# Performance work log

Hardware: AMD Instinct MI355X
Metric: run time of the kernel (lower is better)

The kernel has to match this reference:

```python
import jax, jax.numpy as jnp
import numpy as np

I_CH, O_CH = 64, 64
N_NODES, N_EDGES = 20000, 120000


def build_indices(edge_index):
    """Host-side (numpy) replication of the data-dependent index pipeline:
    sort-by-src -> triplets via searchsorted/repeat_interleave -> sort-by-src ->
    prune low-degree half of nodes -> group-by-src (for scatter-mean) -> reindex.
    All shapes depend only on the (constant) int edge_index.
    """
    ei = np.asarray(edge_index)
    ei = ei[:, np.argsort(ei[0], kind='stable')]
    src, tgt = ei[0], ei[1]
    order = np.argsort(tgt, kind='stable')
    stg = tgt[order]
    lb = np.searchsorted(stg, src, side='left')
    ub = np.searchsorted(stg, src, side='right')
    counts = ub - lb
    T = int(counts.sum())
    rep = np.repeat(np.arange(src.shape[0]), counts)
    start = np.cumsum(counts) - counts
    off = np.arange(T) - start[rep]
    hit = order[lb[rep] + off]
    # triplet rows: (SRC[ALL], TGT[ALL], TGT[R])
    tri = np.stack([src[hit], tgt[hit], tgt[rep]])  # [3, T]
    tri = tri[:, np.argsort(tri[0], kind='stable')]
    # remove(): drop edges touching the lowest-degree half of nodes
    deg = np.bincount(tri.ravel())
    low = np.argsort(deg, kind='stable')[: deg.shape[0] // 2]
    keep = np.ones(deg.shape[0], dtype=bool)
    keep[low] = False
    mask = keep[tri[0]] & keep[tri[1]] & keep[tri[2]]
    pos = np.nonzero(mask)[0]
    tri_kept = tri[:, pos]
    # sum(): group kept triplet-edges by source node
    uniq, inv = np.unique(tri_kept[0], return_inverse=True)
    cnt = np.bincount(inv).astype(np.float32)
    # reindex edge_index to compact node ids
    _, new = np.unique(tri_kept, return_inverse=True)
    new_ei = new.reshape(tri_kept.shape).astype(np.int32)
    return tri.astype(np.int32), pos.astype(np.int32), inv.astype(np.int32), int(uniq.shape[0]), cnt, new_ei


def setup_inputs() -> dict:
    key = jax.random.key(0)
    k1, k2, k3, k4 = jax.random.split(key, 4)
    x = jax.random.normal(k1, (N_NODES, I_CH), dtype=jnp.float32)
    edge_index = jax.random.randint(k2, (2, N_EDGES), 0, N_NODES, dtype=jnp.int32)
    # Conv2d(I, O, (3,1)) parameters
    W = 0.05 * jax.random.normal(k3, (O_CH, I_CH, 3, 1), dtype=jnp.float32)
    b = 0.05 * jax.random.normal(k4, (O_CH,), dtype=jnp.float32)
    return {"x": x, "edge_index": edge_index, "W": W, "b": b}


def reference(x, edge_index, W, b):
    tri, pos, inv, U, cnt, new_ei = build_indices(edge_index)
    tri_j = jnp.asarray(tri)
    # gather: INPUT[i,k,t] = x[tri[k,t], i]  -> g is [3, T, I]
    g = x[tri_j]
    # Conv2d(I,O,(3,1)) on [I,3,T] -> [O,1,T]; squeeze the H dim:
    C = jnp.einsum('oik,kti->ot', W[..., 0], g) + b[:, None]  # [O, T]
    Ck = C[:, jnp.asarray(pos)]  # prune edges touching low-degree nodes
    # scatter-mean over destination group (source node of triplet)
    S = jax.ops.segment_sum(Ck.T, jnp.asarray(inv), num_segments=U)  # [U, O]
    x_new = S / jnp.asarray(cnt)[:, None]
    return x_new, jnp.asarray(new_ei)
```

## Files before the change

kernel.cpp:

```cpp
#include <hip/hip_runtime.h>
#include <stdint.h>

typedef uint32_t u32;
typedef unsigned long long u64;

#define LB_TILE 2048
#define OW_TILE 1024
#define RUN 32

#define S_MAXT 1
#define S_DSTAR 2
#define S_NEED 3
#define S_U 5

__global__ void scan_lb(const u32* __restrict__ in, u32* __restrict__ out, int n,
                        u64* __restrict__ desc){
  __shared__ u32 sh[256];
  __shared__ u32 shPrefix;
  int tid=threadIdx.x, t=blockIdx.x;
  int base = t*LB_TILE + tid*8;
  u32 v[8]; u32 s=0;
#pragma unroll
  for(int k=0;k<8;k++){ u32 xv=(base+k<n)?in[base+k]:0u; v[k]=s; s+=xv; }
  sh[tid]=s; __syncthreads();
  for(int o=1;o<256;o<<=1){
    u32 y=(tid>=o)?sh[tid-o]:0u;
    __syncthreads();
    sh[tid]+=y;
    __syncthreads();
  }
  u32 tileEx = (tid==0)?0u:sh[tid-1];
  u32 agg = sh[255];
  if(tid==0){
    u32 prefix=0u;
    if(t==0){
      atomicExch(&desc[0], ((u64)agg<<32)|2ull);
    } else {
      atomicExch(&desc[t], ((u64)agg<<32)|1ull);
      int j=t-1;
      while(true){
        u64 d=atomicAdd(&desc[j],0ull);
        u32 st=(u32)d;
        if(st==0u) continue;
        prefix += (u32)(d>>32);
        if(st==2u) break;
        --j;
      }
      atomicExch(&desc[t], ((u64)(prefix+agg)<<32)|2ull);
    }
    shPrefix=prefix;
  }
  __syncthreads();
  u32 p=shPrefix+tileEx;
#pragma unroll
  for(int k=0;k<8;k++){ if(base+k<n) out[base+k]=p+v[k]; }
}

__global__ __launch_bounds__(256) void ow_pass(const u64* __restrict__ in,
    u64* __restrict__ outk, const u32* __restrict__ gbase, u64* __restrict__ desc,
    int shift, int hostN, const u32* __restrict__ dCount, int cap){
  __shared__ u32 hist[256], bd[256], cnt2[256];
  __shared__ u32 cnt4[4][256];
  int n = (hostN>=0)?hostN:(int)((*dCount)<(u32)cap?(*dCount):(u32)cap);
  int tid=threadIdx.x, b=blockIdx.x, w=tid>>6, lane=tid&63;
  int base=b*OW_TILE;
  hist[tid]=0u; cnt2[tid]=0u;
  cnt4[0][tid]=0u; cnt4[1][tid]=0u; cnt4[2][tid]=0u; cnt4[3][tid]=0u;
  __syncthreads();
  u64 k[4]; bool act[4];
#pragma unroll
  for(int i=0;i<4;i++){
    int p=base+i*256+tid; act[i]=(p<n);
    k[i]=act[i]?in[p]:0ull;
    if(act[i]) atomicAdd(&hist[(u32)(k[i]>>shift)&255u],1u);
  }
  __syncthreads();
  u32 agg=hist[tid];
  if(b==0){
    atomicExch(&desc[tid], ((u64)agg<<32)|2ull);
    bd[tid]=gbase[tid];
  } else {
    atomicExch(&desc[(size_t)b*256+tid], ((u64)agg<<32)|1ull);
    u32 pre=0u; int j=b-1;
    while(true){
      u64 d=atomicAdd(&desc[(size_t)j*256+tid],0ull);
      u32 st=(u32)d;
      if(st==0u) continue;
      pre+=(u32)(d>>32);
      if(st==2u) break;
      --j;
    }
    atomicExch(&desc[(size_t)b*256+tid], ((u64)(pre+agg)<<32)|2ull);
    bd[tid]=gbase[tid]+pre;
  }
  __syncthreads();
#pragma unroll
  for(int i=0;i<4;i++){
    u32 dig=(u32)(k[i]>>shift)&255u;
    u64 m=__ballot(act[i]?1:0);
    for(int bb=0;bb<8;bb++){
      u64 bl=__ballot((int)((dig>>bb)&1u));
      m &= ((dig>>bb)&1u)?bl:~bl;
    }
    u32 rb=(u32)__popcll(m&((1ull<<lane)-1ull));
    if(act[i]&&rb==0u) cnt4[w][dig]=(u32)__popcll(m);
    __syncthreads();
    if(act[i]){
      u32 off=cnt2[dig]+rb;
      for(int w2=0;w2<w;w2++) off+=cnt4[w2][dig];
      outk[bd[dig]+off]=k[i];
    }
    __syncthreads();
    cnt2[tid]+=cnt4[0][tid]+cnt4[1][tid]+cnt4[2][tid]+cnt4[3][tid];
    cnt4[0][tid]=0u; cnt4[1][tid]=0u; cnt4[2][tid]=0u; cnt4[3][tid]=0u;
    __syncthreads();
  }
}

__global__ void k_prehistE(const u64* __restrict__ keys, u32* __restrict__ hg, int n){
  __shared__ u32 h[4][256];
  int tid=threadIdx.x;
  for(int i=0;i<4;i++) h[i][tid]=0u;
  __syncthreads();
#pragma unroll
  for(int i=0;i<4;i++){
    int p=blockIdx.x*OW_TILE+i*256+tid;
    if(p<n){
      u64 key=keys[p];
      atomicAdd(&h[0][(u32)(key>>24)&255u],1u);
      atomicAdd(&h[1][(u32)(key>>32)&255u],1u);
      atomicAdd(&h[2][(u32)(key>>40)&255u],1u);
      atomicAdd(&h[3][(u32)(key>>48)&255u],1u);
    }
  }
  __syncthreads();
  for(int i=0;i<4;i++) if(h[i][tid]) atomicAdd(&hg[i*256+tid],h[i][tid]);
}

__global__ void k_prehistT(const u64* __restrict__ keys, u32* __restrict__ hg,
                           const u32* __restrict__ dCount, int cap){
  __shared__ u32 h[2][256];
  int n=(int)((*dCount)<(u32)cap?(*dCount):(u32)cap);
  int tid=threadIdx.x;
  h[0][tid]=0u; h[1][tid]=0u;
  __syncthreads();
#pragma unroll
  for(int i=0;i<4;i++){
    int p=blockIdx.x*OW_TILE+i*256+tid;
    if(p<n){
      u64 key=keys[p];
      atomicAdd(&h[0][(u32)(key>>30)&255u],1u);
      atomicAdd(&h[1][(u32)(key>>38)&255u],1u);
    }
  }
  __syncthreads();
  if(h[0][tid]) atomicAdd(&hg[tid],h[0][tid]);
  if(h[1][tid]) atomicAdd(&hg[256+tid],h[1][tid]);
}

__global__ void k_scan256(const u32* __restrict__ hg, u32* __restrict__ gb, int H){
  __shared__ u32 sh[256];
  int t=threadIdx.x;
  for(int hh=0;hh<H;hh++){
    u32 v=hg[hh*256+t];
    sh[t]=v; __syncthreads();
    for(int o=1;o<256;o<<=1){
      u32 y=(t>=o)?sh[t-o]:0u; __syncthreads();
      sh[t]+=y; __syncthreads();
    }
    gb[hh*256+t]=sh[t]-v;
    __syncthreads();
  }
}

__global__ void k_edge0(const u32* __restrict__ src, const u32* __restrict__ tgt,
                        u32* cntS, u32* cntT, u64* keyA, int E){
  int j=blockIdx.x*256+threadIdx.x;
  if(j>=E) return;
  u32 s=src[j], t=tgt[j];
  atomicAdd(&cntS[s],1u); atomicAdd(&cntT[t],1u);
  keyA[j]=((u64)t<<40)|((u64)s<<24)|(u64)j;
}

__global__ void k_deg2m(const u32* __restrict__ src, const u32* __restrict__ tgt,
                        const u32* __restrict__ cntS, const u32* __restrict__ cntT,
                        u32* deg, int* scal, int E){
  __shared__ int mx;
  if(threadIdx.x==0) mx=-1;
  __syncthreads();
  int e=blockIdx.x*256+threadIdx.x;
  int loc=-1;
  if(e<E){
    u32 s=src[e], t=tgt[e];
    u32 w0=cntS[t], w2=cntT[s];
    if(w0){ atomicAdd(&deg[s],w0); loc=(int)(s>t?s:t); }
    if(w2){ atomicAdd(&deg[t],w2); if((int)t>loc) loc=(int)t; }
  }
  if(loc>=0) atomicMax(&mx,loc);
  __syncthreads();
  if(threadIdx.x==0 && mx>=0) atomicMax(&scal[S_MAXT],mx);
}

__global__ void k_degNodeHist(const u32* __restrict__ cntS, const u32* __restrict__ cntT,
                              u32* deg, u32* dh, int NN, const int* __restrict__ scal){
  int v=blockIdx.x*256+threadIdx.x;
  if(v>=NN) return;
  u32 d=deg[v]+cntS[v]*cntT[v];
  deg[v]=d;
  if(v<=scal[S_MAXT]){ if(d>65535u)d=65535u; atomicAdd(&dh[d],1u); }
}

__global__ void k_dstar1b(const u32* __restrict__ dh, int* scal){
  __shared__ u32 part[256];
  __shared__ u32 sc[256];
  int t=threadIdx.x;
  long long kk=(((long long)scal[S_MAXT])+1)>>1;
  u32 s=0;
  for(int i=0;i<256;i++) s+=dh[t*256+i];
  part[t]=s; sc[t]=s; __syncthreads();
  for(int o=1;o<256;o<<=1){
    u32 y=(t>=o)?sc[t-o]:0u; __syncthreads();
    sc[t]+=y; __syncthreads();
  }
  if(kk==0){ if(t==0){ scal[S_DSTAR]=-1; scal[S_NEED]=0; } return; }
  long long cum=(long long)(sc[t]-part[t]);
  if(kk-1>=cum && kk-1<cum+(long long)part[t]){
    long long c=cum;
    for(int i=0;i<256;i++){
      u32 h=dh[t*256+i];
      if(kk-1>=c && kk-1<c+(long long)h){ scal[S_DSTAR]=t*256+i; scal[S_NEED]=(int)(kk-c); break; }
      c+=h;
    }
  }
}

__global__ void k_ef(const u32* __restrict__ deg, u32* ef, int NN, const int* __restrict__ scal){
  int v=blockIdx.x*256+threadIdx.x;
  if(v>NN) return;
  ef[v] = (v<NN && v<=scal[S_MAXT] && (int)deg[v]==scal[S_DSTAR]) ? 1u:0u;
}

__global__ void k_keep(const u32* __restrict__ deg, const u32* __restrict__ rankEq,
                       u32* keep, int NN, const int* __restrict__ scal){
  int v=blockIdx.x*256+threadIdx.x;
  if(v>=NN) return;
  int d=(int)deg[v]; int ds=scal[S_DSTAR]; int need=scal[S_NEED];
  u32 kp=1u;
  if(d<ds) kp=0u;
  else if(d==ds && (int)rankEq[v]<need) kp=0u;
  keep[v]=kp;
}

__global__ void k_keptCnt(const u32* __restrict__ src, const u32* __restrict__ tgt,
                          const u32* __restrict__ keep, u32* kc, int E){
  int j=blockIdx.x*256+threadIdx.x;
  if(j<E && keep[src[j]]) atomicAdd(&kc[tgt[j]],1u);
}

__global__ void k_cntk(const u64* __restrict__ C, const u32* __restrict__ keep,
                       const u32* __restrict__ keptCnt, u32* cntk, int E){
  int e=blockIdx.x*256+threadIdx.x;
  if(e>E) return;
  if(e==E){ cntk[e]=0u; return; }
  u64 ke=C[e];
  u32 s=(u32)(ke>>24)&0xFFFFu, te=(u32)(ke>>40);
  cntk[e]=(keep[s]&keep[te])?keptCnt[s]:0u;
}

__global__ void k_gen_trik(const u64* __restrict__ C, const u64* __restrict__ H,
    const u32* __restrict__ rp_tgt, const u32* __restrict__ keep,
    const u32* __restrict__ startk, u64* __restrict__ trig, int E, int cap){
  int e=blockIdx.x*256+threadIdx.x;
  if(e>=E) return;
  u32 c0=startk[e], c1=startk[e+1];
  if(c0>=c1) return;
  u64 ke=C[e];
  u32 s=(u32)(ke>>24)&0xFFFFu, te=(u32)(ke>>40);
  u32 lb=rp_tgt[s], ub=rp_tgt[s+1];
  u32 idx=c0;
  for(u32 i=lb;i<ub&&idx<c1;++i){
    u64 hk=H[i];
    u32 hsv=(u32)(hk>>24)&0xFFFFu;
    if(keep[hsv]){
      if(idx<(u32)cap) trig[idx]=((u64)hsv<<30)|((u64)s<<15)|(u64)te;
      ++idx;
    }
  }
}

__global__ void k_heads_present(const u64* __restrict__ tri, u32* __restrict__ hf,
    u32* __restrict__ present, const u32* __restrict__ dCount, int KC){
  int Tk=(int)((*dCount)<(u32)KC?(*dCount):(u32)KC);
  int q=blockIdx.x*256+threadIdx.x;
  if(q>KC) return;
  u32 f=0u;
  if(q<Tk){
    u64 key=tri[q];
    f=(q==0||(key>>30)!=(tri[q-1]>>30))?1u:0u;
    present[key>>30]=1u;
    present[(key>>15)&0x7FFFu]=1u;
    present[key&0x7FFFu]=1u;
  }
  hf[q]=f;
}

__global__ void k_gs_ei(const u64* __restrict__ tri, const u32* __restrict__ hf,
    const u32* __restrict__ hsAll, u32* __restrict__ gs, float* __restrict__ out,
    int* scal, const u32* __restrict__ dCount, int KC, int out_size){
  int Tk=(int)((*dCount)<(u32)KC?(*dCount):(u32)KC);
  u32 U=hsAll[KC+1];
  int q=blockIdx.x*256+threadIdx.x;
  if(q==0){ scal[S_U]=(int)U; gs[U]=(u32)Tk; }
  if(q>=Tk) return;
  if(hf[q]) gs[hsAll[q+1]-1u]=(u32)q;
  u64 key=tri[q];
  int bs=(int)U*64;
  int i0=bs+q, i1=bs+Tk+q, i2=bs+2*Tk+q;
  if(i0<out_size) out[i0]=(float)(hsAll[(size_t)KC+1+(size_t)(key>>30)]-U);
  if(i1<out_size) out[i1]=(float)(hsAll[(size_t)KC+1+(size_t)((key>>15)&0x7FFFu)]-U);
  if(i2<out_size) out[i2]=(float)(hsAll[(size_t)KC+1+(size_t)(key&0x7FFFu)]-U);
}

__global__ __launch_bounds__(256) void k_xsum(const float* __restrict__ x,
    const u64* __restrict__ tri, const u32* __restrict__ hs,
    float* __restrict__ S1, float* __restrict__ S2,
    const u32* __restrict__ dCount, int KC){
  int Tk=(int)((*dCount)<(u32)KC?(*dCount):(u32)KC);
  int w=threadIdx.x>>6, lane=threadIdx.x&63;
  int r=blockIdx.x*4+w;
  int q0=r*RUN; if(q0>=Tk) return;
  int q1=q0+RUN; if(q1>Tk)q1=Tk;
  int gcur=(int)hs[q0+1]-1;
  float a1=0.f,a2=0.f;
  for(int q=q0;q<q1;q++){
    int g=(int)hs[q+1]-1;
    if(g!=gcur){
      atomicAdd(&S1[(size_t)gcur*64+lane],a1);
      atomicAdd(&S2[(size_t)gcur*64+lane],a2);
      a1=0.f;a2=0.f;gcur=g;
    }
    u64 key=tri[q];
    a1+=x[(size_t)((key>>15)&0x7FFFull)*64+lane];
    a2+=x[(size_t)(key&0x7FFFull)*64+lane];
  }
  atomicAdd(&S1[(size_t)gcur*64+lane],a1);
  atomicAdd(&S2[(size_t)gcur*64+lane],a2);
}

__global__ __launch_bounds__(256) void k_xmat(const float* __restrict__ x,
    const float* __restrict__ W, const float* __restrict__ b,
    const u64* __restrict__ tri, const u32* __restrict__ gs,
    const float* __restrict__ S1, const float* __restrict__ S2,
    float* __restrict__ out, const int* __restrict__ scal){
  __shared__ float Wl[192*65];
  __shared__ float sv[4][192];
  int tid=threadIdx.x;
  for(int j=tid;j<12288;j+=256){
    int r=j%192, o=j/192;
    Wl[r*65+o]=W[j];
  }
  __syncthreads();
  int U=scal[S_U];
  int w=tid>>6, lane=tid&63;
  float bv=b[lane];
  for(int g=blockIdx.x*4+w; g<U; g+=gridDim.x*4){
    u32 q0=gs[g], q1=gs[g+1];
    u32 uniq=(u32)(tri[q0]>>30);
    sv[w][lane]=x[(size_t)uniq*64+lane];
    sv[w][64+lane]=S1[(size_t)g*64+lane];
    sv[w][128+lane]=S2[(size_t)g*64+lane];
    float acc0=0.f, acc12=0.f;
#pragma unroll 4
    for(int ii=0;ii<64;ii++){
      acc0  += Wl[(ii*3+0)*65+lane]*sv[w][ii];
      acc12 += Wl[(ii*3+1)*65+lane]*sv[w][64+ii]
             + Wl[(ii*3+2)*65+lane]*sv[w][128+ii];
    }
    out[(size_t)g*64+lane] = bv + acc0 + acc12/(float)(q1-q0);
  }
}

extern "C" void kernel_launch(void* const* d_in, const int* in_sizes, int n_in,
                              void* d_out, int out_size, void* d_ws, size_t ws_size,
                              hipStream_t stream){
  const float* x = (const float*)d_in[0];
  const int*   ei = (const int*)d_in[1];
  const float* W = (const float*)d_in[2];
  const float* b = (const float*)d_in[3];
  int NN = in_sizes[0]/64;
  int E  = in_sizes[1]/2;
  const u32* src=(const u32*)ei;
  const u32* tgt=(const u32*)(ei+E);

  int KC = ((out_size/3 + OW_TILE-1)/OW_TILE)*OW_TILE; if(KC<OW_TILE) KC=OW_TILE;
  int B_E=(E+OW_TILE-1)/OW_TILE;
  int B_T=KC/OW_TILE;

  char* base=(char*)d_ws; size_t off=0;
  auto alloc=[&](size_t nInts)->u32*{
    u32* p=(u32*)(base+off);
    off += ( (nInts*4 + 255) & ~(size_t)255 );
    return p;
  };
  int* scal=(int*)alloc(64);
  u32* cntT=alloc(NN+1); u32* cntS=alloc(NN);
  u32* deg=alloc(NN); u32* degHist=alloc(65536);
  u32* keptCnt=alloc(NN);
  u32* histGE=alloc(4*256); u32* histGT=alloc(2*256);
  u64* descS=(u64*)alloc(2*1024);
  u64* descE=(u64*)alloc(2*(size_t)(4*B_E*256));
  u64* descT=(u64*)alloc(2*(size_t)(2*B_T*256));
  u32* hfp=alloc((size_t)KC+1+NN+1);
  float* S1=(float*)alloc((size_t)NN*64);
  float* S2=(float*)alloc((size_t)NN*64);
  size_t zoneBytes = off;
  u64* bufA=(u64*)alloc(2*(size_t)E);
  u64* bufB=(u64*)alloc(2*(size_t)E);
  u64* bufC=(u64*)alloc(2*(size_t)E);
  u64* triA=(u64*)alloc(2*(size_t)KC); u64* triB=(u64*)alloc(2*(size_t)KC);
  u32* rp_tgt=alloc(NN+1);
  u32* cntk=alloc(E+1); u32* startk=alloc(E+1);
  u32* gbaseE=alloc(4*256); u32* gbaseT=alloc(2*256);
  u32* ef=alloc(NN+1); u32* rankEq=alloc(NN+1); u32* keep=alloc(NN);
  u32* gs=alloc(NN+2);
  u32* hsAll=alloc((size_t)KC+1+NN+1);
  if(off > ws_size) return;

  u32* hf=hfp; u32* present=hfp+(KC+1);
  const u32* dCount=startk+E;

  size_t descUsed=0;
  auto scan_ex=[&](const u32* in, u32* out, int n){
    int nb=(n+LB_TILE-1)/LB_TILE;
    scan_lb<<<nb,256,0,stream>>>(in,out,n,descS+descUsed);
    descUsed += (size_t)nb;
  };

  int gE=(E+255)/256, gE1=(E+256)/256;
  int gNN=(NN+255)/256, gNN1=(NN+256)/256;
  int gKC=(KC+255)/256, gKC1=(KC+256)/256;

  hipMemsetAsync(base,0,zoneBytes,stream);

  k_edge0<<<gE,256,0,stream>>>(src,tgt,cntS,cntT,bufA,E);
  k_deg2m<<<gE,256,0,stream>>>(src,tgt,cntS,cntT,deg,scal,E);
  k_degNodeHist<<<gNN,256,0,stream>>>(cntS,cntT,deg,degHist,NN,scal);
  k_dstar1b<<<1,256,0,stream>>>(degHist,scal);
  k_ef<<<gNN1,256,0,stream>>>(deg,ef,NN,scal);
  scan_ex(ef,rankEq,NN+1);
  k_keep<<<gNN,256,0,stream>>>(deg,rankEq,keep,NN,scal);
  k_keptCnt<<<gE,256,0,stream>>>(src,tgt,keep,keptCnt,E);
  scan_ex(cntT,rp_tgt,NN+1);

  k_prehistE<<<B_E,256,0,stream>>>(bufA,histGE,E);
  k_scan256<<<1,256,0,stream>>>(histGE,gbaseE,4);
  ow_pass<<<B_E,256,0,stream>>>(bufA,bufB,gbaseE+0*256,descE+(size_t)0*B_E*256,24,E,nullptr,0);
  ow_pass<<<B_E,256,0,stream>>>(bufB,bufC,gbaseE+1*256,descE+(size_t)1*B_E*256,32,E,nullptr,0);
  ow_pass<<<B_E,256,0,stream>>>(bufC,bufA,gbaseE+2*256,descE+(size_t)2*B_E*256,40,E,nullptr,0);
  ow_pass<<<B_E,256,0,stream>>>(bufA,bufB,gbaseE+3*256,descE+(size_t)3*B_E*256,48,E,nullptr,0);

  k_cntk<<<gE1,256,0,stream>>>(bufC,keep,keptCnt,cntk,E);
  scan_ex(cntk,startk,E+1);
  k_gen_trik<<<gE,256,0,stream>>>(bufC,bufB,rp_tgt,keep,startk,triA,E,KC);

  k_prehistT<<<B_T,256,0,stream>>>(triA,histGT,dCount,KC);
  k_scan256<<<1,256,0,stream>>>(histGT,gbaseT,2);
  ow_pass<<<B_T,256,0,stream>>>(triA,triB,gbaseT+0*256,descT+(size_t)0*B_T*256,30,-1,dCount,KC);
  ow_pass<<<B_T,256,0,stream>>>(triB,triA,gbaseT+1*256,descT+(size_t)1*B_T*256,38,-1,dCount,KC);

  k_heads_present<<<gKC1,256,0,stream>>>(triA,hf,present,dCount,KC);
  scan_ex(hfp,hsAll,KC+1+NN+1);
  float* outF=(float*)d_out;
  k_gs_ei<<<gKC,256,0,stream>>>(triA,hf,hsAll,gs,outF,scal,dCount,KC,out_size);

  k_xsum<<<KC/(4*RUN),256,0,stream>>>(x,triA,hsAll,S1,S2,dCount,KC);
  k_xmat<<<768,256,0,stream>>>(x,W,b,triA,gs,S1,S2,outF,scal);
}
```

Before: 337.3 us.

## Shrink edge sort keys to 32 bits and derive radix bases from degree counts

Edge sort keys are packed as 32-bit (src<<16|tgt) instead of 64-bit keys that carried the edge index, which halves traffic in the four edge radix passes. Global digit bases come from the per-node src/tgt counts via a new k_gbase4 kernel, and the triplet histogram is built inside k_gen_trik, so the separate prehistogram kernels are dropped. The two exclusive scans are merged into one over a concatenated buffer, and radix and scan tiles grow to 4096 elements per block. The trade-offs are that edge order becomes non-stable (the index is no longer in the key), node ids must fit in 16 bits, and larger tiles mean fewer blocks and more registers per thread.

```diff
diff --git a/kernel.cpp b/kernel.cpp
--- a/kernel.cpp
+++ b/kernel.cpp
@@ -4,8 +4,8 @@
 typedef uint32_t u32;
 typedef unsigned long long u64;
 
-#define LB_TILE 2048
-#define OW_TILE 1024
+#define LB_TILE 4096
+#define OW_TILE 4096
 #define RUN 32
 
 #define S_MAXT 1
@@ -18,10 +18,10 @@
   __shared__ u32 sh[256];
   __shared__ u32 shPrefix;
   int tid=threadIdx.x, t=blockIdx.x;
-  int base = t*LB_TILE + tid*8;
-  u32 v[8]; u32 s=0;
+  int base = t*LB_TILE + tid*16;
+  u32 v[16]; u32 s=0;
 #pragma unroll
-  for(int k=0;k<8;k++){ u32 xv=(base+k<n)?in[base+k]:0u; v[k]=s; s+=xv; }
+  for(int k=0;k<16;k++){ u32 xv=(base+k<n)?in[base+k]:0u; v[k]=s; s+=xv; }
   sh[tid]=s; __syncthreads();
   for(int o=1;o<256;o<<=1){
     u32 y=(tid>=o)?sh[tid-o]:0u;
@@ -53,26 +53,25 @@
   __syncthreads();
   u32 p=shPrefix+tileEx;
 #pragma unroll
-  for(int k=0;k<8;k++){ if(base+k<n) out[base+k]=p+v[k]; }
-}
-
-__global__ __launch_bounds__(256) void ow_pass(const u64* __restrict__ in,
-    u64* __restrict__ outk, const u32* __restrict__ gbase, u64* __restrict__ desc,
-    int shift, int hostN, const u32* __restrict__ dCount, int cap){
+  for(int k=0;k<16;k++){ if(base+k<n) out[base+k]=p+v[k]; }
+}
+
+__global__ __launch_bounds__(256) void ow32(const u32* __restrict__ in,
+    u32* __restrict__ outk, const u32* __restrict__ gbase, u64* __restrict__ desc,
+    int shift, int n){
   __shared__ u32 hist[256], bd[256], cnt2[256];
   __shared__ u32 cnt4[4][256];
-  int n = (hostN>=0)?hostN:(int)((*dCount)<(u32)cap?(*dCount):(u32)cap);
   int tid=threadIdx.x, b=blockIdx.x, w=tid>>6, lane=tid&63;
   int base=b*OW_TILE;
   hist[tid]=0u; cnt2[tid]=0u;
   cnt4[0][tid]=0u; cnt4[1][tid]=0u; cnt4[2][tid]=0u; cnt4[3][tid]=0u;
   __syncthreads();
-  u64 k[4]; bool act[4];
+  u32 k[16]; bool act[16];
 #pragma unroll
-  for(int i=0;i<4;i++){
+  for(int i=0;i<16;i++){
     int p=base+i*256+tid; act[i]=(p<n);
-    k[i]=act[i]?in[p]:0ull;
-    if(act[i]) atomicAdd(&hist[(u32)(k[i]>>shift)&255u],1u);
+    k[i]=act[i]?in[p]:0u;
+    if(act[i]) atomicAdd(&hist[(k[i]>>shift)&255u],1u);
   }
   __syncthreads();
   u32 agg=hist[tid];
@@ -95,7 +94,69 @@
   }
   __syncthreads();
 #pragma unroll
-  for(int i=0;i<4;i++){
+  for(int i=0;i<16;i++){
+    u32 dig=(k[i]>>shift)&255u;
+    u64 m=__ballot(act[i]?1:0);
+    for(int bb=0;bb<8;bb++){
+      u64 bl=__ballot((int)((dig>>bb)&1u));
+      m &= ((dig>>bb)&1u)?bl:~bl;
+    }
+    u32 rb=(u32)__popcll(m&((1ull<<lane)-1ull));
+    if(act[i]&&rb==0u) cnt4[w][dig]=(u32)__popcll(m);
+    __syncthreads();
+    if(act[i]){
+      u32 off=cnt2[dig]+rb;
+      for(int w2=0;w2<w;w2++) off+=cnt4[w2][dig];
+      u32 pos=bd[dig]+off;
+      if(pos<(u32)n) outk[pos]=k[i];
+    }
+    __syncthreads();
+    cnt2[tid]+=cnt4[0][tid]+cnt4[1][tid]+cnt4[2][tid]+cnt4[3][tid];
+    cnt4[0][tid]=0u; cnt4[1][tid]=0u; cnt4[2][tid]=0u; cnt4[3][tid]=0u;
+    __syncthreads();
+  }
+}
+
+__global__ __launch_bounds__(256) void ow64(const u64* __restrict__ in,
+    u64* __restrict__ outk, const u32* __restrict__ gbase, u64* __restrict__ desc,
+    int shift, const u32* __restrict__ dCount, int cap){
+  __shared__ u32 hist[256], bd[256], cnt2[256];
+  __shared__ u32 cnt4[4][256];
+  int n=(int)((*dCount)<(u32)cap?(*dCount):(u32)cap);
+  int tid=threadIdx.x, b=blockIdx.x, w=tid>>6, lane=tid&63;
+  int base=b*OW_TILE;
+  hist[tid]=0u; cnt2[tid]=0u;
+  cnt4[0][tid]=0u; cnt4[1][tid]=0u; cnt4[2][tid]=0u; cnt4[3][tid]=0u;
+  __syncthreads();
+  u64 k[16]; bool act[16];
+#pragma unroll
+  for(int i=0;i<16;i++){
+    int p=base+i*256+tid; act[i]=(p<n);
+    k[i]=act[i]?in[p]:0ull;
+    if(act[i]) atomicAdd(&hist[(u32)(k[i]>>shift)&255u],1u);
+  }
+  __syncthreads();
+  u32 agg=hist[tid];
+  if(b==0){
+    atomicExch(&desc[tid], ((u64)agg<<32)|2ull);
+    bd[tid]=gbase[tid];
+  } else {
+    atomicExch(&desc[(size_t)b*256+tid], ((u64)agg<<32)|1ull);
+    u32 pre=0u; int j=b-1;
+    while(true){
+      u64 d=atomicAdd(&desc[(size_t)j*256+tid],0ull);
+      u32 st=(u32)d;
+      if(st==0u) continue;
+      pre+=(u32)(d>>32);
+      if(st==2u) break;
+      --j;
+    }
+    atomicExch(&desc[(size_t)b*256+tid], ((u64)(pre+agg)<<32)|2ull);
+    bd[tid]=gbase[tid]+pre;
+  }
+  __syncthreads();
+#pragma unroll
+  for(int i=0;i<16;i++){
     u32 dig=(u32)(k[i]>>shift)&255u;
     u64 m=__ballot(act[i]?1:0);
     for(int bb=0;bb<8;bb++){
@@ -108,7 +169,8 @@
     if(act[i]){
       u32 off=cnt2[dig]+rb;
       for(int w2=0;w2<w;w2++) off+=cnt4[w2][dig];
-      outk[bd[dig]+off]=k[i];
+      u32 pos=bd[dig]+off;
+      if(pos<(u32)n) outk[pos]=k[i];
     }
     __syncthreads();
     cnt2[tid]+=cnt4[0][tid]+cnt4[1][tid]+cnt4[2][tid]+cnt4[3][tid];
@@ -117,69 +179,13 @@
   }
 }
 
-__global__ void k_prehistE(const u64* __restrict__ keys, u32* __restrict__ hg, int n){
-  __shared__ u32 h[4][256];
-  int tid=threadIdx.x;
-  for(int i=0;i<4;i++) h[i][tid]=0u;
-  __syncthreads();
-#pragma unroll
-  for(int i=0;i<4;i++){
-    int p=blockIdx.x*OW_TILE+i*256+tid;
-    if(p<n){
-      u64 key=keys[p];
-      atomicAdd(&h[0][(u32)(key>>24)&255u],1u);
-      atomicAdd(&h[1][(u32)(key>>32)&255u],1u);
-      atomicAdd(&h[2][(u32)(key>>40)&255u],1u);
-      atomicAdd(&h[3][(u32)(key>>48)&255u],1u);
-    }
-  }
-  __syncthreads();
-  for(int i=0;i<4;i++) if(h[i][tid]) atomicAdd(&hg[i*256+tid],h[i][tid]);
-}
-
-__global__ void k_prehistT(const u64* __restrict__ keys, u32* __restrict__ hg,
-                           const u32* __restrict__ dCount, int cap){
-  __shared__ u32 h[2][256];
-  int n=(int)((*dCount)<(u32)cap?(*dCount):(u32)cap);
-  int tid=threadIdx.x;
-  h[0][tid]=0u; h[1][tid]=0u;
-  __syncthreads();
-#pragma unroll
-  for(int i=0;i<4;i++){
-    int p=blockIdx.x*OW_TILE+i*256+tid;
-    if(p<n){
-      u64 key=keys[p];
-      atomicAdd(&h[0][(u32)(key>>30)&255u],1u);
-      atomicAdd(&h[1][(u32)(key>>38)&255u],1u);
-    }
-  }
-  __syncthreads();
-  if(h[0][tid]) atomicAdd(&hg[tid],h[0][tid]);
-  if(h[1][tid]) atomicAdd(&hg[256+tid],h[1][tid]);
-}
-
-__global__ void k_scan256(const u32* __restrict__ hg, u32* __restrict__ gb, int H){
-  __shared__ u32 sh[256];
-  int t=threadIdx.x;
-  for(int hh=0;hh<H;hh++){
-    u32 v=hg[hh*256+t];
-    sh[t]=v; __syncthreads();
-    for(int o=1;o<256;o<<=1){
-      u32 y=(t>=o)?sh[t-o]:0u; __syncthreads();
-      sh[t]+=y; __syncthreads();
-    }
-    gb[hh*256+t]=sh[t]-v;
-    __syncthreads();
-  }
-}
-
 __global__ void k_edge0(const u32* __restrict__ src, const u32* __restrict__ tgt,
-                        u32* cntS, u32* cntT, u64* keyA, int E){
+                        u32* cntS, u32* cntT, u32* keyA, int E){
   int j=blockIdx.x*256+threadIdx.x;
   if(j>=E) return;
   u32 s=src[j], t=tgt[j];
   atomicAdd(&cntS[s],1u); atomicAdd(&cntT[t],1u);
-  keyA[j]=((u64)t<<40)|((u64)s<<24)|(u64)j;
+  keyA[j]=(s<<16)|t;
 }
 
 __global__ void k_deg2m(const u32* __restrict__ src, const u32* __restrict__ tgt,
@@ -257,35 +263,81 @@
   if(j<E && keep[src[j]]) atomicAdd(&kc[tgt[j]],1u);
 }
 
-__global__ void k_cntk(const u64* __restrict__ C, const u32* __restrict__ keep,
+__global__ void k_gbase4(const u32* __restrict__ cntS, const u32* __restrict__ cntT,
+                         u32* __restrict__ gbase, int NN){
+  __shared__ u32 sh[256];
+  int p=blockIdx.x, d=threadIdx.x;
+  const u32* c=(p<2)?cntS:cntT;
+  u32 s=0;
+  if((p&1)==0){ for(int i=d;i<NN;i+=256) s+=c[i]; }
+  else { int s0=d*256, s1=s0+256; if(s1>NN)s1=NN; for(int i=s0;i<s1;i++) s+=c[i]; }
+  sh[d]=s; __syncthreads();
+  for(int o=1;o<256;o<<=1){
+    u32 y=(d>=o)?sh[d-o]:0u; __syncthreads();
+    sh[d]+=y; __syncthreads();
+  }
+  gbase[p*256+d]=sh[d]-s;
+}
+
+__global__ void k_scan256(const u32* __restrict__ hg, u32* __restrict__ gb, int H){
+  __shared__ u32 sh[256];
+  int t=threadIdx.x;
+  for(int hh=0;hh<H;hh++){
+    u32 v=hg[hh*256+t];
+    sh[t]=v; __syncthreads();
+    for(int o=1;o<256;o<<=1){
+      u32 y=(t>=o)?sh[t-o]:0u; __syncthreads();
+      sh[t]+=y; __syncthreads();
+    }
+    gb[hh*256+t]=sh[t]-v;
+    __syncthreads();
+  }
+}
+
+__global__ void k_cntk(const u32* __restrict__ C, const u32* __restrict__ keep,
                        const u32* __restrict__ keptCnt, u32* cntk, int E){
   int e=blockIdx.x*256+threadIdx.x;
   if(e>E) return;
   if(e==E){ cntk[e]=0u; return; }
-  u64 ke=C[e];
-  u32 s=(u32)(ke>>24)&0xFFFFu, te=(u32)(ke>>40);
+  u32 ke=C[e];
+  u32 s=ke>>16, te=ke&0xFFFFu;
   cntk[e]=(keep[s]&keep[te])?keptCnt[s]:0u;
 }
 
-__global__ void k_gen_trik(const u64* __restrict__ C, const u64* __restrict__ H,
-    const u32* __restrict__ rp_tgt, const u32* __restrict__ keep,
-    const u32* __restrict__ startk, u64* __restrict__ trig, int E, int cap){
-  int e=blockIdx.x*256+threadIdx.x;
-  if(e>=E) return;
-  u32 c0=startk[e], c1=startk[e+1];
-  if(c0>=c1) return;
-  u64 ke=C[e];
-  u32 s=(u32)(ke>>24)&0xFFFFu, te=(u32)(ke>>40);
-  u32 lb=rp_tgt[s], ub=rp_tgt[s+1];
-  u32 idx=c0;
-  for(u32 i=lb;i<ub&&idx<c1;++i){
-    u64 hk=H[i];
-    u32 hsv=(u32)(hk>>24)&0xFFFFu;
-    if(keep[hsv]){
-      if(idx<(u32)cap) trig[idx]=((u64)hsv<<30)|((u64)s<<15)|(u64)te;
-      ++idx;
-    }
-  }
+__global__ void k_gen_trik(const u32* __restrict__ C, const u32* __restrict__ H,
+    const u32* __restrict__ rp, const u32* __restrict__ keep,
+    const u32* __restrict__ startk, u64* __restrict__ trig, u32* __restrict__ histGT,
+    int E, int cap){
+  __shared__ u32 h0[256], h1[256];
+  int tid=threadIdx.x;
+  h0[tid]=0u; h1[tid]=0u;
+  __syncthreads();
+  int e=blockIdx.x*256+tid;
+  if(e<E){
+    u32 c0=startk[e], c1=startk[e+1];
+    if(c0<c1){
+      u32 ke=C[e];
+      u32 s=ke>>16, te=ke&0xFFFFu;
+      u32 r0=rp[0];
+      u32 lb=rp[s]-r0, ub=rp[s+1]-r0;
+      u32 idx=c0;
+      for(u32 i=lb;i<ub&&idx<c1;++i){
+        u32 hsv=H[i]>>16;
+        if(keep[hsv]){
+          if(idx<(u32)cap){
+            u64 key=((u64)hsv<<30)|((u64)s<<15)|(u64)te;
+            trig[idx]=key;
+            atomicAdd(&h0[(u32)(key>>30)&255u],1u);
+            atomicAdd(&h1[(u32)(key>>38)&255u],1u);
+          }
+          ++idx;
+        }
+      }
+    }
+  }
+  __syncthreads();
+  if(h0[tid]) atomicAdd(&histGT[tid],h0[tid]);
+  if(h1[tid]) atomicAdd(&histGT[256+tid],h1[tid]);
 }
 
 __global__ void k_heads_present(const u64* __restrict__ tri, u32* __restrict__ hf,
@@ -403,10 +455,11 @@
     return p;
   };
   int* scal=(int*)alloc(64);
-  u32* cntT=alloc(NN+1); u32* cntS=alloc(NN);
+  u32* cntS=alloc(NN);
   u32* deg=alloc(NN); u32* degHist=alloc(65536);
   u32* keptCnt=alloc(NN);
-  u32* histGE=alloc(4*256); u32* histGT=alloc(2*256);
+  u32* histGT=alloc(2*256);
+  u32* catA=alloc(2*(size_t)(NN+1));
   u64* descS=(u64*)alloc(2*1024);
   u64* descE=(u64*)alloc(2*(size_t)(4*B_E*256));
   u64* descT=(u64*)alloc(2*(size_t)(2*B_T*256));
@@ -414,18 +467,18 @@
   float* S1=(float*)alloc((size_t)NN*64);
   float* S2=(float*)alloc((size_t)NN*64);
   size_t zoneBytes = off;
-  u64* bufA=(u64*)alloc(2*(size_t)E);
-  u64* bufB=(u64*)alloc(2*(size_t)E);
-  u64* bufC=(u64*)alloc(2*(size_t)E);
+  u32* ebA=alloc(E); u32* ebB=alloc(E); u32* ebC=alloc(E);
   u64* triA=(u64*)alloc(2*(size_t)KC); u64* triB=(u64*)alloc(2*(size_t)KC);
-  u32* rp_tgt=alloc(NN+1);
   u32* cntk=alloc(E+1); u32* startk=alloc(E+1);
+  u32* catB=alloc(2*(size_t)(NN+1));
   u32* gbaseE=alloc(4*256); u32* gbaseT=alloc(2*256);
-  u32* ef=alloc(NN+1); u32* rankEq=alloc(NN+1); u32* keep=alloc(NN);
+  u32* keep=alloc(NN);
   u32* gs=alloc(NN+2);
   u32* hsAll=alloc((size_t)KC+1+NN+1);
   if(off > ws_size) return;
 
+  u32* ef=catA; u32* cntT=catA+(NN+1);
+  u32* rankEq=catB; u32* rp=catB+(NN+1);
   u32* hf=hfp; u32* present=hfp+(KC+1);
   const u32* dCount=startk+E;
 
@@ -442,31 +495,28 @@
 
   hipMemsetAsync(base,0,zoneBytes,stream);
 
-  k_edge0<<<gE,256,0,stream>>>(src,tgt,cntS,cntT,bufA,E);
+  k_edge0<<<gE,256,0,stream>>>(src,tgt,cntS,cntT,ebA,E);
   k_deg2m<<<gE,256,0,stream>>>(src,tgt,cntS,cntT,deg,scal,E);
   k_degNodeHist<<<gNN,256,0,stream>>>(cntS,cntT,deg,degHist,NN,scal);
   k_dstar1b<<<1,256,0,stream>>>(degHist,scal);
   k_ef<<<gNN1,256,0,stream>>>(deg,ef,NN,scal);
-  scan_ex(ef,rankEq,NN+1);
+  scan_ex(catA,catB,2*(NN+1));
   k_keep<<<gNN,256,0,stream>>>(deg,rankEq,keep,NN,scal);
   k_keptCnt<<<gE,256,0,stream>>>(src,tgt,keep,keptCnt,E);
-  scan_ex(cntT,rp_tgt,NN+1);
-
-  k_prehistE<<<B_E,256,0,stream>>>(bufA,histGE,E);
-  k_scan256<<<1,256,0,stream>>>(histGE,gbaseE,4);
-  ow_pass<<<B_E,256,0,stream>>>(bufA,bufB,gbaseE+0*256,descE+(size_t)0*B_E*256,24,E,nullptr,0);
-  ow_pass<<<B_E,256,0,stream>>>(bufB,bufC,gbaseE+1*256,descE+(size_t)1*B_E*256,32,E,nullptr,0);
-  ow_pass<<<B_E,256,0,stream>>>(bufC,bufA,gbaseE+2*256,descE+(size_t)2*B_E*256,40,E,nullptr,0);
-  ow_pass<<<B_E,256,0,stream>>>(bufA,bufB,gbaseE+3*256,descE+(size_t)3*B_E*256,48,E,nullptr,0);
-
-  k_cntk<<<gE1,256,0,stream>>>(bufC,keep,keptCnt,cntk,E);
+
+  k_gbase4<<<4,256,0,stream>>>(cntS,cntT,gbaseE,NN);
+  ow32<<<B_E,256,0,stream>>>(ebA,ebB,gbaseE+0*256,descE+(size_t)0*B_E*256,16,E);
+  ow32<<<B_E,256,0,stream>>>(ebB,ebC,gbaseE+1*256,descE+(size_t)1*B_E*256,24,E);
+  ow32<<<B_E,256,0,stream>>>(ebC,ebA,gbaseE+2*256,descE+(size_t)2*B_E*256,0,E);
+  ow32<<<B_E,256,0,stream>>>(ebA,ebB,gbaseE+3*256,descE+(size_t)3*B_E*256,8,E);
+
+  k_cntk<<<gE1,256,0,stream>>>(ebC,keep,keptCnt,cntk,E);
   scan_ex(cntk,startk,E+1);
-  k_gen_trik<<<gE,256,0,stream>>>(bufC,bufB,rp_tgt,keep,startk,triA,E,KC);
-
-  k_prehistT<<<B_T,256,0,stream>>>(triA,histGT,dCount,KC);
+  k_gen_trik<<<gE,256,0,stream>>>(ebC,ebB,rp,keep,startk,triA,histGT,E,KC);
+
   k_scan256<<<1,256,0,stream>>>(histGT,gbaseT,2);
-  ow_pass<<<B_T,256,0,stream>>>(triA,triB,gbaseT+0*256,descT+(size_t)0*B_T*256,30,-1,dCount,KC);
-  ow_pass<<<B_T,256,0,stream>>>(triB,triA,gbaseT+1*256,descT+(size_t)1*B_T*256,38,-1,dCount,KC);
+  ow64<<<B_T,256,0,stream>>>(triA,triB,gbaseT+0*256,descT+(size_t)0*B_T*256,30,dCount,KC);
+  ow64<<<B_T,256,0,stream>>>(triB,triA,gbaseT+1*256,descT+(size_t)1*B_T*256,38,dCount,KC);
 
   k_heads_present<<<gKC1,256,0,stream>>>(triA,hf,present,dCount,KC);
   scan_ex(hfp,hsAll,KC+1+NN+1);
```

Result: slower. 373.1 us (+10.6%).
